# Optimization experiments

Hardware: AMD Instinct MI355X
Metric: run time of the kernel (lower is better)

The kernel has to match this reference:

```python
import jax, jax.numpy as jnp
import numpy as np

K = 5  # k_for_maxpool
EPS_OH = 1.0 - 0.001


def _conv_block(x, W, b):
    # x: [N, L, D]; Conv1d(D, D, 3, padding=2), LeakyReLU(0.1), slice [1:1+L], residual
    L = x.shape[1]
    xc = jnp.swapaxes(x, 1, 2)  # [N, D, L]
    y = jax.lax.conv_general_dilated(xc, W, window_strides=(1,), padding=[(2, 2)],
                                     dimension_numbers=('NCH', 'OIH', 'NCH'))
    y = y + b[None, :, None]
    y = jax.nn.leaky_relu(y, 0.1)
    y = y[:, :, 1:1 + L]
    return jnp.swapaxes(y, 1, 2) + x


def _normalize(x):
    return x / jnp.linalg.norm(x, axis=-1, keepdims=True)


def _pool(sim):
    # sim: [..., Q, L] -> [..., Q, 3]: (max, mean of top-K, mean over all)
    s = jnp.sort(sim, axis=-1)
    kmax = s[..., -K:]
    return jnp.stack([kmax[..., -1], kmax.mean(-1), s.mean(-1)], axis=-1)


def setup_inputs() -> dict:
    key = jax.random.key(0)
    ks = jax.random.split(key, 16)
    S, L, Q, D = 4096, 64, 32, 300
    inp = {
        'doc_sents_embeds': jax.random.normal(ks[0], (S, L, D), jnp.float32),
        'question_embeds': jax.random.normal(ks[1], (Q, D), jnp.float32),
        'q_idfs': jax.random.uniform(ks[2], (Q, 1), jnp.float32),
        'sents_gaf': jax.random.uniform(ks[3], (S, 3), jnp.float32),
        'conv1_w': jax.random.normal(ks[4], (D, D, 3), jnp.float32) * 0.05,
        'conv1_b': jax.random.normal(ks[5], (D,), jnp.float32) * 0.05,
        'conv2_w': jax.random.normal(ks[6], (D, D, 3), jnp.float32) * 0.05,
        'conv2_b': jax.random.normal(ks[7], (D,), jnp.float32) * 0.05,
        'qw_w': jax.random.normal(ks[8], (1, D + 1), jnp.float32) * 0.05,
        'qw_b': jax.random.normal(ks[9], (1,), jnp.float32) * 0.05,
        'mlp1_w': jax.random.normal(ks[10], (8, 9), jnp.float32) * 0.3,
        'mlp1_b': jax.random.normal(ks[11], (8,), jnp.float32) * 0.05,
        'mlp2_w': jax.random.normal(ks[12], (1, 8), jnp.float32) * 0.3,
        'mlp2_b': jax.random.normal(ks[13], (1,), jnp.float32) * 0.05,
        'out_w': jax.random.normal(ks[14], (1, 4), jnp.float32) * 0.3,
    }
    return inp


def reference(doc_sents_embeds, question_embeds, q_idfs, sents_gaf,
              conv1_w, conv1_b, conv2_w, conv2_b,
              qw_w, qw_b, mlp1_w, mlp1_b, mlp2_w, mlp2_b, out_w):
    Q = question_embeds.shape[0]
    # question context (two trigram conv blocks)
    q_ctx = _conv_block(_conv_block(question_embeds[None], conv1_w, conv1_b),
                        conv2_w, conv2_b)[0]  # [Q, D]
    # question token weights
    qw_in = jnp.concatenate([q_ctx, q_idfs], axis=-1)  # [Q, D+1]
    q_weights = jax.nn.softmax((qw_in @ qw_w.T + qw_b)[:, 0], axis=-1)  # [Q]
    # sentence context features, vectorized over all sentences
    sent_ctx = _conv_block(_conv_block(doc_sents_embeds, conv1_w, conv1_b),
                           conv2_w, conv2_b)  # [S, L, D]
    # cosine similarity matrices: [S, Q, L]
    qn = _normalize(question_embeds)
    dn = _normalize(doc_sents_embeds)
    sim_insens = jnp.einsum('qd,sld->sql', qn, dn)
    sim_oh = (sim_insens > EPS_OH).astype(sim_insens.dtype)
    qcn = _normalize(q_ctx)
    scn = _normalize(sent_ctx)
    sim_sens = jnp.einsum('qd,sld->sql', qcn, scn)
    # pooled features: [S, Q, 9] (order: oh, insensitive, sensitive)
    pooled = jnp.concatenate([_pool(sim_oh), _pool(sim_insens), _pool(sim_sens)], axis=-1)
    lo = jax.nn.leaky_relu(pooled @ mlp1_w.T + mlp1_b, 0.1)
    lo = (lo @ mlp2_w.T + mlp2_b)[..., 0]  # [S, Q]
    sent_emit = (lo * q_weights[None, :]).sum(-1) / Q  # [S]
    feats = jnp.concatenate([sents_gaf, sent_emit[:, None]], axis=-1)  # [S, 4]
    return jax.nn.sigmoid(feats @ out_w[0])  # [S]
```

## Files before the change

### kernel.cpp

```cpp
#include <hip/hip_runtime.h>
#include <math.h>

typedef __attribute__((ext_vector_type(8))) short short8;
typedef __attribute__((ext_vector_type(4))) short short4_t;
typedef __attribute__((ext_vector_type(4))) float f32x4;

#define RS      312
#define SST     69
#define EPS_OH  0.999f

__device__ __forceinline__ float waveSum(float v) {
#pragma unroll
  for (int off = 32; off; off >>= 1) v += __shfl_xor(v, off);
  return v;
}
__device__ __forceinline__ float leaky(float x) { return fmaxf(x, 0.1f * x); }

__device__ __forceinline__ short f2b(float f) {
  unsigned u = __float_as_uint(f);
  unsigned r = (u + 0x7FFFu + ((u >> 16) & 1u)) >> 16;
  return (short)r;
}
__device__ __forceinline__ float b2f(short h) {
  return __uint_as_float(((unsigned)(unsigned short)h) << 16);
}

__global__ __launch_bounds__(256) void qconv_kernel(
    const float* __restrict__ x, const float* __restrict__ W,
    const float* __restrict__ b, float* __restrict__ y)
{
  int idx = blockIdx.x * 256 + threadIdx.x;
  if (idx >= 76800) return;
  int part = idx & 7, gid = idx >> 3;
  int o = gid % 300, l = gid / 300;
  const float* Wo = W + o * 900;
  float acc = 0.f;
  for (int i = part; i < 300; i += 8) {
    float x1 = x[l * 300 + i];
    float x0 = (l >= 1) ? x[(l - 1) * 300 + i] : 0.f;
    float x2 = (l <= 30) ? x[(l + 1) * 300 + i] : 0.f;
    acc += Wo[i * 3] * x0 + Wo[i * 3 + 1] * x1 + Wo[i * 3 + 2] * x2;
  }
  acc += __shfl_xor(acc, 1);
  acc += __shfl_xor(acc, 2);
  acc += __shfl_xor(acc, 4);
  if (part == 0) y[gid] = leaky(acc + b[o]) + x[gid];
}

__global__ __launch_bounds__(256) void qfinish_kernel(
    const float* __restrict__ qemb, const float* __restrict__ qctx,
    const float* __restrict__ qidf, const float* __restrict__ qww,
    const float* __restrict__ qwb,
    float* __restrict__ qwv, short* __restrict__ qf)
{
  __shared__ float inq[32], inqc[32], lg[32];
  int tid = threadIdx.x, lane = tid & 63, w = tid >> 6;
  int r = w * 8 + (lane >> 3), sub = lane & 7;
  float sq = 0.f, sqc = 0.f, dt = 0.f;
  for (int i = sub; i < 300; i += 8) {
    float a = qemb[r * 300 + i]; sq  += a * a;
    float c = qctx[r * 300 + i]; sqc += c * c;
    dt += c * qww[i];
  }
#pragma unroll
  for (int off = 4; off; off >>= 1) {
    sq  += __shfl_xor(sq, off);
    sqc += __shfl_xor(sqc, off);
    dt  += __shfl_xor(dt, off);
  }
  if (sub == 0) {
    inq[r] = rsqrtf(sq); inqc[r] = rsqrtf(sqc);
    lg[r] = dt + qidf[r] * qww[300] + qwb[0];
  }
  __syncthreads();
  if (w == 0) {
    float L = (lane < 32) ? lg[lane] : -1e30f;
    float m = L;
#pragma unroll
    for (int off = 32; off; off >>= 1) m = fmaxf(m, __shfl_xor(m, off));
    float e = (lane < 32) ? expf(L - m) : 0.f;
    float ssum = e;
#pragma unroll
    for (int off = 32; off; off >>= 1) ssum += __shfl_xor(ssum, off);
    if (lane < 32) qwv[lane] = e / ssum;
  }
  __syncthreads();
  for (int t = tid; t < 2560; t += 256) {
    int ln = t & 63;
    int rest = t >> 6;
    int kt = rest % 10; rest /= 10;
    int mt = rest & 1; int sflag = rest >> 1;
    const float* src  = sflag ? qctx : qemb;
    const float* innv = sflag ? inqc : inq;
    int q  = mt * 16 + (ln & 15);
    int i0 = kt * 32 + (ln >> 4) * 8;
    float iv = innv[q];
    short8 v;
#pragma unroll
    for (int j = 0; j < 8; ++j) {
      int i = i0 + j;
      v[j] = f2b((i < 300) ? src[q * 300 + i] * iv : 0.f);
    }
    *(short8*)(qf + (size_t)t * 8) = v;
  }
}

__global__ __launch_bounds__(256) void wfrag_kernel(
    const float* __restrict__ W, short* __restrict__ Wf)
{
  int t = blockIdx.x * 256 + threadIdx.x;
  if (t >= 38400) return;
  int lane = t & 63;
  int rest = t >> 6;
  int mt = rest % 20; rest /= 20;
  int kt = rest % 10; int tap = rest / 10;
  int o  = mt * 16 + (lane & 15);
  int i0 = kt * 32 + (lane >> 4) * 8;
  short8 v;
#pragma unroll
  for (int j = 0; j < 8; ++j) {
    int i = i0 + j;
    v[j] = f2b((o < 300 && i < 300) ? W[o * 900 + i * 3 + tap] : 0.f);
  }
  *(short8*)(Wf + (size_t)t * 8) = v;
}


__device__ __forceinline__ void pool_all(
    const float* SIMb, float* featb, int lane, int foff, bool do_oh)
{
  int q = lane >> 1, half = lane & 1;
  const float* p = SIMb + q * SST + half * 32;
  float t0 = -3e38f, t1 = -3e38f, t2 = -3e38f, t3 = -3e38f, t4 = -3e38f;
  float ssum = 0.f;
  int cnt = 0;
#pragma unroll
  for (int i = 0; i < 32; ++i) {
    float v = p[i];
    ssum += v;
    if (do_oh) cnt += (v > EPS_OH) ? 1 : 0;
    float m, c;
    m = fmaxf(t0, v); c = fminf(t0, v); t0 = m;
    m = fmaxf(t1, c); c = fminf(t1, c); t1 = m;
    m = fmaxf(t2, c); c = fminf(t2, c); t2 = m;
    m = fmaxf(t3, c); c = fminf(t3, c); t3 = m;
    t4 = fmaxf(t4, c);
  }
  float p0 = __shfl_xor(t0, 1), p1 = __shfl_xor(t1, 1), p2 = __shfl_xor(t2, 1),
        p3 = __shfl_xor(t3, 1), p4 = __shfl_xor(t4, 1);
  float s2 = __shfl_xor(ssum, 1);
  int   c2 = __shfl_xor(cnt, 1);
  float m0 = fmaxf(t0, p4), m1 = fmaxf(t1, p3), m2 = fmaxf(t2, p2),
        m3 = fmaxf(t3, p1), m4 = fmaxf(t4, p0);
  if (half == 0) {
    float tmax = fmaxf(t0, p0);
    float t5   = m0 + m1 + m2 + m3 + m4;
    float stot = ssum + s2;
    int   c    = cnt + c2;
    float* fq = featb + q * 9;
    if (do_oh) {
      fq[0] = (c > 0) ? 1.f : 0.f;
      fq[1] = (c < 5 ? (float)c : 5.f) * 0.2f;
      fq[2] = (float)c * (1.f / 64.f);
    }
    fq[foff + 0] = tmax;
    fq[foff + 1] = t5 * 0.2f;
    fq[foff + 2] = stot * (1.f / 64.f);
  }
}

__device__ __forceinline__ void conv_mfma_ip2(
    short* tb, const short* __restrict__ Wf,
    const float* __restrict__ bias, int w, int r, int g, int lane)
{
  f32x4 acc[2][4];
#pragma unroll
  for (int mi = 0; mi < 2; ++mi)
#pragma unroll
    for (int nt = 0; nt < 4; ++nt) acc[mi][nt] = (f32x4){0.f, 0.f, 0.f, 0.f};

  const int rm0 = (r == 0) ? 0 : (r - 1);
  const int rp3 = (r == 15) ? 63 : (49 + r);
  const short* wl = Wf + (size_t)lane * 8;

#pragma unroll
  for (int kt = 0; kt < 10; ++kt) {
    const int koff = kt * 32 + g * 8;
    short8 bf[3][4];
#pragma unroll
    for (int tap = 0; tap < 3; ++tap) {
#pragma unroll
      for (int nt = 0; nt < 4; ++nt) {
        int l = nt * 16 + r;
        int rowi = (tap == 0) ? ((nt == 0) ? rm0 : (l - 1))
                 : (tap == 1) ? l
                              : ((nt == 3) ? rp3 : (l + 1));
        bf[tap][nt] = *(const short8*)(tb + rowi * RS + koff);
      }
    }
    bf[0][0] = (r == 0)  ? (short8)0 : bf[0][0];
    bf[2][3] = (r == 15) ? (short8)0 : bf[2][3];
#pragma unroll
    for (int tap = 0; tap < 3; ++tap) {
#pragma unroll
      for (int mi = 0; mi < 2; ++mi) {
        const int mt = w * 2 + mi;
        short8 af = *(const short8*)(wl + (size_t)((tap * 10 + kt) * 20 + mt) * 512);
#pragma unroll
        for (int nt = 0; nt < 4; ++nt)
          acc[mi][nt] = __builtin_amdgcn_mfma_f32_16x16x32_bf16(af, bf[tap][nt], acc[mi][nt], 0, 0, 0);
      }
    }
  }
  f32x4 bv[2];
  short4_t resv[2][4];
#pragma unroll
  for (int mi = 0; mi < 2; ++mi) {
    const int m0 = (w * 2 + mi) * 16 + g * 4;
    if (m0 < 300) {
      bv[mi] = *(const f32x4*)(bias + m0);
#pragma unroll
      for (int nt = 0; nt < 4; ++nt)
        resv[mi][nt] = *(const short4_t*)(tb + (nt * 16 + r) * RS + m0);
    }
  }
  __syncthreads();
#pragma unroll
  for (int mi = 0; mi < 2; ++mi) {
    const int m0 = (w * 2 + mi) * 16 + g * 4;
    if (m0 < 300) {
#pragma unroll
      for (int nt = 0; nt < 4; ++nt) {
        int l = nt * 16 + r;
        short4_t outv;
#pragma unroll
        for (int j = 0; j < 4; ++j) {
          float a = acc[mi][nt][j] + bv[mi][j];
          a = leaky(a) + b2f(resv[mi][nt][j]);
          outv[j] = f2b(a);
        }
        *(short4_t*)(tb + l * RS + m0) = outv;
      }
    }
  }
}

__device__ __forceinline__ void sim_mfma(
    const short* src, const short* __restrict__ qf, const float* invn,
    float* SIMb, int ti, int r, int g, int lane)
{
  int smt = ti >> 2, snt = ti & 3;
  f32x4 acc = (f32x4){0.f, 0.f, 0.f, 0.f};
#pragma unroll
  for (int kt = 0; kt < 10; ++kt) {
    short8 bf = *(const short8*)(src + (snt * 16 + r) * RS + kt * 32 + g * 8);
    short8 af = *(const short8*)(qf + (size_t)((smt * 10 + kt) * 64 + lane) * 8);
    acc = __builtin_amdgcn_mfma_f32_16x16x32_bf16(af, bf, acc, 0, 0, 0);
  }
  int l = snt * 16 + r;
  float iv = invn[l];
#pragma unroll
  for (int j = 0; j < 4; ++j)
    SIMb[(smt * 16 + g * 4 + j) * SST + l] = acc[j] * iv;
}

__device__ __forceinline__ void norms_lds(const short* Xb, float* invn, int tid) {
  if (tid >= 512) return;
  int row = tid >> 3, part = tid & 7;
  float ssum = 0.f;
  for (int i = part * 8; i < 304; i += 64) {
    short8 hv = *(const short8*)(Xb + row * RS + i);
#pragma unroll
    for (int j = 0; j < 8; ++j) { float f = b2f(hv[j]); ssum += f * f; }
  }
  ssum += __shfl_xor(ssum, 1);
  ssum += __shfl_xor(ssum, 2);
  ssum += __shfl_xor(ssum, 4);
  if (part == 0) invn[row] = rsqrtf(ssum);
}

__global__ __launch_bounds__(640, 5) void sent_kernel(
    const float* __restrict__ doc, const short* __restrict__ qf,
    const float* __restrict__ qwv, const float* __restrict__ gaf,
    const short* __restrict__ Wf1, const float* __restrict__ b1,
    const short* __restrict__ Wf2, const float* __restrict__ b2,
    const float* __restrict__ m1w, const float* __restrict__ m1b,
    const float* __restrict__ m2w, const float* __restrict__ m2b,
    const float* __restrict__ ow, float* __restrict__ out)
{
  __shared__ short TB[64 * RS + 8];
  __shared__ float SIMb[32 * SST];
  __shared__ float invn[64];
  __shared__ float featb[288];

  const int tid = threadIdx.x, lane = tid & 63, w = tid >> 6;
  const int r = lane & 15, g = lane >> 4;
  const int s = blockIdx.x;

  if (tid >= 576) {
    short* p = TB + (tid - 576) * RS + 300;
    *(short4_t*)p = (short4_t)0;
    *(short8*)(p + 4) = (short8)0;
  } else if (tid == 575) {
    *(short8*)(TB + 64 * RS) = (short8)0;
  }
  if (tid < 512) {
    int l = tid >> 3, part = tid & 7;
    const float* xr = doc + (size_t)s * 19200 + l * 300;
    float ssum = 0.f;
#pragma unroll
    for (int m = 0; m < 5; ++m) {
      int c = part * 8 + m * 64;
      if (c <= 292) {
        f32x4 u0 = *(const f32x4*)(xr + c);
        f32x4 u1 = *(const f32x4*)(xr + c + 4);
        short8 o;
#pragma unroll
        for (int j = 0; j < 4; ++j) {
          ssum += u0[j] * u0[j] + u1[j] * u1[j];
          o[j] = f2b(u0[j]); o[4 + j] = f2b(u1[j]);
        }
        *(short8*)(TB + l * RS + c) = o;
      } else if (c == 296) {
        f32x4 u0 = *(const f32x4*)(xr + 296);
        short4_t o;
#pragma unroll
        for (int j = 0; j < 4; ++j) { ssum += u0[j] * u0[j]; o[j] = f2b(u0[j]); }
        *(short4_t*)(TB + l * RS + 296) = o;
      }
    }
    ssum += __shfl_xor(ssum, 1);
    ssum += __shfl_xor(ssum, 2);
    ssum += __shfl_xor(ssum, 4);
    if (part == 0) invn[l] = rsqrtf(ssum);
  }
  __syncthreads();

  if (w < 8) sim_mfma(TB, qf, invn, SIMb, w, r, g, lane);
  __syncthreads();

  if (w == 8) pool_all(SIMb, featb, lane, 3, true);
  __syncthreads();

  conv_mfma_ip2(TB, Wf1, b1, w, r, g, lane);
  __syncthreads();

  conv_mfma_ip2(TB, Wf2, b2, w, r, g, lane);
  __syncthreads();

  norms_lds(TB, invn, tid);
  __syncthreads();

  if (w < 8) sim_mfma(TB, qf + 10240, invn, SIMb, w, r, g, lane);
  __syncthreads();

  if (w == 9) pool_all(SIMb, featb, lane, 6, false);
  __syncthreads();

  if (w == 0) {
    float val = 0.f;
    if (lane < 32) {
      int q = lane;
      float o8 = m2b[0];
#pragma unroll
      for (int j = 0; j < 8; ++j) {
        float a = m1b[j];
#pragma unroll
        for (int f = 0; f < 9; ++f) a += m1w[j * 9 + f] * featb[q * 9 + f];
        a = leaky(a);
        o8 += m2w[j] * a;
      }
      val = o8 * qwv[q];
    }
    float tot = waveSum(val);
    if (lane == 0) {
      float emit = tot * (1.f / 32.f);
      float z = gaf[s * 3 + 0] * ow[0] + gaf[s * 3 + 1] * ow[1] +
                gaf[s * 3 + 2] * ow[2] + emit * ow[3];
      out[s] = 1.f / (1.f + expf(-z));
    }
  }
}

extern "C" void kernel_launch(void* const* d_in, const int* in_sizes, int n_in,
                              void* d_out, int out_size, void* d_ws, size_t ws_size,
                              hipStream_t stream)
{
  const float* doc  = (const float*)d_in[0];
  const float* qemb = (const float*)d_in[1];
  const float* qidf = (const float*)d_in[2];
  const float* gaf  = (const float*)d_in[3];
  const float* W1   = (const float*)d_in[4];
  const float* b1   = (const float*)d_in[5];
  const float* W2   = (const float*)d_in[6];
  const float* b2   = (const float*)d_in[7];
  const float* qww  = (const float*)d_in[8];
  const float* qwb  = (const float*)d_in[9];
  const float* m1w  = (const float*)d_in[10];
  const float* m1b  = (const float*)d_in[11];
  const float* m2w  = (const float*)d_in[12];
  const float* m2b  = (const float*)d_in[13];
  const float* ow   = (const float*)d_in[14];
  float* out = (float*)d_out;

  float* ws   = (float*)d_ws;
  float* qc1  = ws;
  float* qctx = ws + 9600;
  float* qwv  = ws + 19200;
  short* wsS  = (short*)(ws + 19232);
  short* Wf1  = wsS;
  short* Wf2  = wsS + 307200;
  short* qfS  = wsS + 614400;

  wfrag_kernel<<<150, 256, 0, stream>>>(W1, Wf1);
  wfrag_kernel<<<150, 256, 0, stream>>>(W2, Wf2);
  qconv_kernel<<<300, 256, 0, stream>>>(qemb, W1, b1, qc1);
  qconv_kernel<<<300, 256, 0, stream>>>(qc1, W2, b2, qctx);
  qfinish_kernel<<<1, 256, 0, stream>>>(qemb, qctx, qidf, qww, qwb, qwv, qfS);
  sent_kernel<<<4096, 640, 0, stream>>>(doc, qfS, qwv, gaf, Wf1, b1, Wf2, b2,
                                        m1w, m1b, m2w, m2b, ow, out);
}
```

Baseline: 563.4 us.

## Shrink sentence block to 8 waves and move row-norm scaling into pooling

The sentence kernel now runs 512 threads (8 waves) instead of 640, and the 20 conv M-tiles are split unevenly: the first three waves take 3 tiles each, the rest take 2. The inverse-norm scaling moves from the similarity MFMA epilogue into the pooling pass. This removes one barrier between the row-norm computation and the second similarity GEMM. The goal is to cut idle waves and one sync per block. The trade-off is load imbalance in the conv phase and more accumulator registers in the 3-tile waves.

```diff
diff --git a/kernel.cpp b/kernel.cpp
--- a/kernel.cpp
+++ b/kernel.cpp
@@ -127,16 +127,18 @@
 
 
 __device__ __forceinline__ void pool_all(
-    const float* SIMb, float* featb, int lane, int foff, bool do_oh)
+    const float* SIMb, const float* invn, float* featb,
+    int lane, int foff, bool do_oh)
 {
   int q = lane >> 1, half = lane & 1;
-  const float* p = SIMb + q * SST + half * 32;
+  const float* p  = SIMb + q * SST + half * 32;
+  const float* iv = invn + half * 32;
   float t0 = -3e38f, t1 = -3e38f, t2 = -3e38f, t3 = -3e38f, t4 = -3e38f;
   float ssum = 0.f;
   int cnt = 0;
 #pragma unroll
   for (int i = 0; i < 32; ++i) {
-    float v = p[i];
+    float v = p[i] * iv[i];
     ssum += v;
     if (do_oh) cnt += (v > EPS_OH) ? 1 : 0;
     float m, c;
@@ -169,19 +171,20 @@
   }
 }
 
-__device__ __forceinline__ void conv_mfma_ip2(
+template <int NMT>
+__device__ __forceinline__ void conv_ip(
     short* tb, const short* __restrict__ Wf,
-    const float* __restrict__ bias, int w, int r, int g, int lane)
-{
-  f32x4 acc[2][4];
-#pragma unroll
-  for (int mi = 0; mi < 2; ++mi)
+    const float* __restrict__ bias, int base, int r, int g, int lane)
+{
+  f32x4 acc[NMT][4];
+#pragma unroll
+  for (int mi = 0; mi < NMT; ++mi)
 #pragma unroll
     for (int nt = 0; nt < 4; ++nt) acc[mi][nt] = (f32x4){0.f, 0.f, 0.f, 0.f};
 
   const int rm0 = (r == 0) ? 0 : (r - 1);
   const int rp3 = (r == 15) ? 63 : (49 + r);
-  const short* wl = Wf + (size_t)lane * 8;
+  const short* wl = Wf + (size_t)lane * 8 + (size_t)base * 512;
 
 #pragma unroll
   for (int kt = 0; kt < 10; ++kt) {
@@ -203,20 +206,19 @@
 #pragma unroll
     for (int tap = 0; tap < 3; ++tap) {
 #pragma unroll
-      for (int mi = 0; mi < 2; ++mi) {
-        const int mt = w * 2 + mi;
-        short8 af = *(const short8*)(wl + (size_t)((tap * 10 + kt) * 20 + mt) * 512);
+      for (int mi = 0; mi < NMT; ++mi) {
+        short8 af = *(const short8*)(wl + (size_t)((tap * 10 + kt) * 20 + mi) * 512);
 #pragma unroll
         for (int nt = 0; nt < 4; ++nt)
           acc[mi][nt] = __builtin_amdgcn_mfma_f32_16x16x32_bf16(af, bf[tap][nt], acc[mi][nt], 0, 0, 0);
       }
     }
   }
-  f32x4 bv[2];
-  short4_t resv[2][4];
-#pragma unroll
-  for (int mi = 0; mi < 2; ++mi) {
-    const int m0 = (w * 2 + mi) * 16 + g * 4;
+  f32x4 bv[NMT];
+  short4_t resv[NMT][4];
+#pragma unroll
+  for (int mi = 0; mi < NMT; ++mi) {
+    const int m0 = (base + mi) * 16 + g * 4;
     if (m0 < 300) {
       bv[mi] = *(const f32x4*)(bias + m0);
 #pragma unroll
@@ -226,8 +228,8 @@
   }
   __syncthreads();
 #pragma unroll
-  for (int mi = 0; mi < 2; ++mi) {
-    const int m0 = (w * 2 + mi) * 16 + g * 4;
+  for (int mi = 0; mi < NMT; ++mi) {
+    const int m0 = (base + mi) * 16 + g * 4;
     if (m0 < 300) {
 #pragma unroll
       for (int nt = 0; nt < 4; ++nt) {
@@ -246,8 +248,8 @@
 }
 
 __device__ __forceinline__ void sim_mfma(
-    const short* src, const short* __restrict__ qf, const float* invn,
-    float* SIMb, int ti, int r, int g, int lane)
+    const short* src, const short* __restrict__ qf, float* SIMb,
+    int ti, int r, int g, int lane)
 {
   int smt = ti >> 2, snt = ti & 3;
   f32x4 acc = (f32x4){0.f, 0.f, 0.f, 0.f};
@@ -258,14 +260,12 @@
     acc = __builtin_amdgcn_mfma_f32_16x16x32_bf16(af, bf, acc, 0, 0, 0);
   }
   int l = snt * 16 + r;
-  float iv = invn[l];
 #pragma unroll
   for (int j = 0; j < 4; ++j)
-    SIMb[(smt * 16 + g * 4 + j) * SST + l] = acc[j] * iv;
+    SIMb[(smt * 16 + g * 4 + j) * SST + l] = acc[j];
 }
 
 __device__ __forceinline__ void norms_lds(const short* Xb, float* invn, int tid) {
-  if (tid >= 512) return;
   int row = tid >> 3, part = tid & 7;
   float ssum = 0.f;
   for (int i = part * 8; i < 304; i += 64) {
@@ -279,7 +279,7 @@
   if (part == 0) invn[row] = rsqrtf(ssum);
 }
 
-__global__ __launch_bounds__(640, 5) void sent_kernel(
+__global__ __launch_bounds__(512, 4) void sent_kernel(
     const float* __restrict__ doc, const short* __restrict__ qf,
     const float* __restrict__ qwv, const float* __restrict__ gaf,
     const short* __restrict__ Wf1, const float* __restrict__ b1,
@@ -297,14 +297,13 @@
   const int r = lane & 15, g = lane >> 4;
   const int s = blockIdx.x;
 
-  if (tid >= 576) {
-    short* p = TB + (tid - 576) * RS + 300;
+  if (tid < 64) {
+    short* p = TB + tid * RS + 300;
     *(short4_t*)p = (short4_t)0;
     *(short8*)(p + 4) = (short8)0;
-  } else if (tid == 575) {
-    *(short8*)(TB + 64 * RS) = (short8)0;
-  }
-  if (tid < 512) {
+    if (tid == 0) *(short8*)(TB + 64 * RS) = (short8)0;
+  }
+  {
     int l = tid >> 3, part = tid & 7;
     const float* xr = doc + (size_t)s * 19200 + l * 300;
     float ssum = 0.f;
@@ -336,25 +335,25 @@
   }
   __syncthreads();
 
-  if (w < 8) sim_mfma(TB, qf, invn, SIMb, w, r, g, lane);
-  __syncthreads();
-
-  if (w == 8) pool_all(SIMb, featb, lane, 3, true);
-  __syncthreads();
-
-  conv_mfma_ip2(TB, Wf1, b1, w, r, g, lane);
-  __syncthreads();
-
-  conv_mfma_ip2(TB, Wf2, b2, w, r, g, lane);
+  sim_mfma(TB, qf, SIMb, w, r, g, lane);
+  __syncthreads();
+
+  if (w == 6) pool_all(SIMb, invn, featb, lane, 3, true);
+  __syncthreads();
+
+  if (w < 3) conv_ip<3>(TB, Wf1, b1, 3 * w, r, g, lane);
+  else       conv_ip<2>(TB, Wf1, b1, 2 * w + 3, r, g, lane);
+  __syncthreads();
+
+  if (w < 3) conv_ip<3>(TB, Wf2, b2, 3 * w, r, g, lane);
+  else       conv_ip<2>(TB, Wf2, b2, 2 * w + 3, r, g, lane);
   __syncthreads();
 
   norms_lds(TB, invn, tid);
-  __syncthreads();
-
-  if (w < 8) sim_mfma(TB, qf + 10240, invn, SIMb, w, r, g, lane);
-  __syncthreads();
-
-  if (w == 9) pool_all(SIMb, featb, lane, 6, false);
+  sim_mfma(TB, qf + 10240, SIMb, w, r, g, lane);
+  __syncthreads();
+
+  if (w == 7) pool_all(SIMb, invn, featb, lane, 6, false);
   __syncthreads();
 
   if (w == 0) {
@@ -417,6 +416,6 @@
   qconv_kernel<<<300, 256, 0, stream>>>(qemb, W1, b1, qc1);
   qconv_kernel<<<300, 256, 0, stream>>>(qc1, W2, b2, qctx);
   qfinish_kernel<<<1, 256, 0, stream>>>(qemb, qctx, qidf, qww, qwb, qwv, qfS);
-  sent_kernel<<<4096, 640, 0, stream>>>(doc, qfS, qwv, gaf, Wf1, b1, Wf2, b2,
+  sent_kernel<<<4096, 512, 0, stream>>>(doc, qfS, qwv, gaf, Wf1, b1, Wf2, b2,
                                         m1w, m1b, m2w, m2b, ow, out);
 }
```

New measurement: 588.0 us. +4.4%, slower.
